# Kernel optimization log

Hardware: AMD Instinct MI355X
Metric: run time of the kernel (lower is better)

The kernel has to match this reference:

```python
import jax, jax.numpy as jnp
import numpy as np

NUM_RELS = 1315
FEAT_DIM = 768
RD = 32  # rel_emb_dim
OD = 32  # out_dim
B = 65536  # entities per side
NNZ = 1048576  # nonzeros per incidence matrix (avg degree 16)
EPS = 1e-12  # torch F.normalize eps


def _normalize(x):
    n = jnp.linalg.norm(x, axis=1, keepdims=True)
    return x / jnp.maximum(n, EPS)


def _agg(rows, cols, vals, rel_emb):
    # sparse.mm(inc, rel_emb): gather rel rows, scale, scatter-add to entities -> [B, RD]
    return jax.ops.segment_sum(vals[:, None] * rel_emb[cols], rows, num_segments=B)


def _entity_emb(ri, ci, vi, ro, co, vo, feat, rel_emb, W_in, b_in, W_out, b_out, W_ent, b_ent):
    in_emb = _agg(ri, ci, vi, rel_emb) @ W_in.T + b_in
    out_emb = _agg(ro, co, vo, rel_emb) @ W_out.T + b_out
    f = jnp.concatenate([feat, in_emb, out_emb], axis=1)  # [B, FEAT+2*RD]
    return _normalize(f @ W_ent.T + b_ent)


def setup_inputs() -> dict:
    key = jax.random.key(0)
    ks = iter(jax.random.split(key, 40))
    d = {}
    for p in ("h", "pos_t", "neg_t"):
        for s in ("in", "out"):
            d[f"{p}_{s}_rows"] = jax.random.randint(next(ks), (NNZ,), 0, B, dtype=jnp.int32)
            d[f"{p}_{s}_cols"] = jax.random.randint(next(ks), (NNZ,), 0, NUM_RELS, dtype=jnp.int32)
            d[f"{p}_{s}_vals"] = jax.random.uniform(next(ks), (NNZ,), dtype=jnp.float32)
        d[f"{p}_node_feat"] = jax.random.normal(next(ks), (B, FEAT_DIM), dtype=jnp.float32)
    d["eid"] = jax.random.randint(next(ks), (B,), 0, NUM_RELS, dtype=jnp.int32)
    # learned parameters
    d["rel_emb"] = jax.random.normal(next(ks), (NUM_RELS, RD), dtype=jnp.float32) * 0.02
    d["W_in"] = jax.random.normal(next(ks), (RD, RD), dtype=jnp.float32) * 0.1
    d["b_in"] = jnp.zeros((RD,), dtype=jnp.float32)
    d["W_out"] = jax.random.normal(next(ks), (RD, RD), dtype=jnp.float32) * 0.1
    d["b_out"] = jnp.zeros((RD,), dtype=jnp.float32)
    d["W_ent"] = jax.random.normal(next(ks), (OD, FEAT_DIM + 2 * RD), dtype=jnp.float32) * 0.02
    d["b_ent"] = jnp.zeros((OD,), dtype=jnp.float32)
    d["W_rel"] = jax.random.normal(next(ks), (OD, RD), dtype=jnp.float32) * 0.1
    d["b_rel"] = jnp.zeros((OD,), dtype=jnp.float32)
    return d


def reference(h_in_rows, h_in_cols, h_in_vals, h_out_rows, h_out_cols, h_out_vals, h_node_feat,
              pos_t_in_rows, pos_t_in_cols, pos_t_in_vals, pos_t_out_rows, pos_t_out_cols, pos_t_out_vals, pos_t_node_feat,
              neg_t_in_rows, neg_t_in_cols, neg_t_in_vals, neg_t_out_rows, neg_t_out_cols, neg_t_out_vals, neg_t_node_feat,
              eid, rel_emb, W_in, b_in, W_out, b_out, W_ent, b_ent, W_rel, b_rel):
    r_emb = _normalize(rel_emb[eid] @ W_rel.T + b_rel)  # [B, OD]
    h_emb = _entity_emb(h_in_rows, h_in_cols, h_in_vals, h_out_rows, h_out_cols, h_out_vals,
                        h_node_feat, rel_emb, W_in, b_in, W_out, b_out, W_ent, b_ent)
    pos_t_emb = _entity_emb(pos_t_in_rows, pos_t_in_cols, pos_t_in_vals, pos_t_out_rows, pos_t_out_cols, pos_t_out_vals,
                            pos_t_node_feat, rel_emb, W_in, b_in, W_out, b_out, W_ent, b_ent)
    neg_t_emb = _entity_emb(neg_t_in_rows, neg_t_in_cols, neg_t_in_vals, neg_t_out_rows, neg_t_out_cols, neg_t_out_vals,
                            neg_t_node_feat, rel_emb, W_in, b_in, W_out, b_out, W_ent, b_ent)
    pos_score = jnp.linalg.norm(h_emb + r_emb - pos_t_emb, axis=1)
    neg_score = jnp.linalg.norm(h_emb + r_emb - neg_t_emb, axis=1)
    return (pos_score, neg_score)
```

## Files before the change

### kernel.cpp

```cpp
#include <hip/hip_runtime.h>
#include <math.h>

#define N_RELS 1315
#define NB 65536
#define NNZV (1 << 20)
#define FEATD 768

#define NBUK 256
#define CAP  4608
#define CHUNK 4096
#define STG  2048
#define EPT  8
#define FPT  9

typedef float f32x4 __attribute__((ext_vector_type(4)));
typedef short s16x8 __attribute__((ext_vector_type(8)));
typedef float v2f  __attribute__((ext_vector_type(2)));

struct Mats { const int* rows[6]; const int* cols[6]; const float* vals[6]; };

__device__ __forceinline__ short f2bf(float f) {
    return __builtin_bit_cast(short, (__bf16)f);
}

__global__ void k_prep(const float* __restrict__ rel_emb,
                       const float* __restrict__ W_in, const float* __restrict__ b_in,
                       const float* __restrict__ W_out, const float* __restrict__ b_out,
                       const float* __restrict__ W_ent, const float* __restrict__ b_ent,
                       const float* __restrict__ W_rel, const float* __restrict__ b_rel,
                       float* __restrict__ Pcat, float* __restrict__ Prel,
                       float* __restrict__ bprime, unsigned* __restrict__ cursor)
{
    __shared__ float C[2][32][33];
    const int tid = threadIdx.x;
    if (cursor != nullptr && blockIdx.x < 6) {
        const int i = blockIdx.x * 256 + tid;
        cursor[i] = (unsigned)i * CAP;
    }
    for (int idx = tid; idx < 2 * 32 * 32; idx += 256) {
        int d = idx >> 10, o = (idx >> 5) & 31, t = idx & 31;
        const float* W  = d ? W_out : W_in;
        const float* we = W_ent + o * 832 + 768 + d * 32;
        float s = 0.f;
        #pragma unroll
        for (int j = 0; j < 32; ++j) s += we[j] * W[j * 32 + t];
        C[d][o][t] = s;
    }
    __syncthreads();

    const int row8 = blockIdx.x * 8 + (tid >> 5);
    const int o = tid & 31;
    if (row8 < 2 * N_RELS) {
        const int d = (row8 >= N_RELS) ? 1 : 0;
        const int r = row8 - d * N_RELS;
        const float* re = rel_emb + r * 32;
        float s = 0.f;
        #pragma unroll
        for (int t = 0; t < 32; ++t) s += re[t] * C[d][o][t];
        Pcat[row8 * 32 + o] = s;
    } else if (row8 < 3 * N_RELS) {
        const int r = row8 - 2 * N_RELS;
        const float* re = rel_emb + r * 32;
        float s = b_rel[o];
        #pragma unroll
        for (int j = 0; j < 32; ++j) s += W_rel[o * 32 + j] * re[j];
        float sq = s * s;
        #pragma unroll
        for (int m = 16; m; m >>= 1) sq += __shfl_xor(sq, m);
        Prel[r * 32 + o] = s / fmaxf(sqrtf(sq), 1e-12f);
    }
    if (blockIdx.x == 0 && tid < 32) {
        float s = b_ent[tid];
        #pragma unroll
        for (int j = 0; j < 32; ++j)
            s += b_in[j] * W_ent[tid * 832 + 768 + j] + b_out[j] * W_ent[tid * 832 + 800 + j];
        bprime[tid] = s;
    }
}

__global__ void k_wfrag(const float* __restrict__ W_ent, s16x8* __restrict__ wsB)
{
    const int t = blockIdx.x * 256 + threadIdx.x;
    if (t >= 24 * 2 * 64) return;
    const int kk = t >> 7, rem = t & 127, nt = rem >> 6, l = rem & 63;
    const int col = nt * 16 + (l & 15);
    const int k0  = kk * 32 + ((l >> 4) << 3);
    const float* w = W_ent + col * 832 + k0;
    s16x8 v;
    #pragma unroll
    for (int e = 0; e < 8; ++e) v[e] = f2bf(w[e]);
    wsB[t] = v;
}

__global__ __launch_bounds__(256) void k_bin(Mats m, uint2* __restrict__ bins,
                                             unsigned* __restrict__ cursor)
{
    __shared__ unsigned lcnt[NBUK];
    __shared__ unsigned gbase[NBUK];
    const int mm    = blockIdx.x >> 8;
    const int chunk = blockIdx.x & 255;
    const int tid   = threadIdx.x;
    const int* __restrict__ R = m.rows[mm];
    const int* __restrict__ C = m.cols[mm];
    const float* __restrict__ V = m.vals[mm];
    const int base = chunk * CHUNK;

    for (int st = 0; st < CHUNK / STG; ++st) {
        for (int i = tid; i < NBUK; i += 256) lcnt[i] = 0;
        __syncthreads();
        unsigned meta[EPT]; float val[EPT]; unsigned short lrank[EPT]; unsigned char buk[EPT];
        #pragma unroll
        for (int e = 0; e < EPT; ++e) {
            const int idx = base + st * STG + e * 256 + tid;
            const int row = R[idx];
            const int col = C[idx];
            val[e]  = V[idx];
            buk[e]  = (unsigned char)(row >> 8);
            meta[e] = ((unsigned)(row & 255) << 11) | (unsigned)col;
            lrank[e] = (unsigned short)atomicAdd(&lcnt[buk[e]], 1u);
        }
        __syncthreads();
        gbase[tid] = atomicAdd(&cursor[mm * NBUK + tid], lcnt[tid]);
        __syncthreads();
        #pragma unroll
        for (int e = 0; e < EPT; ++e)
            bins[gbase[buk[e]] + lrank[e]] = make_uint2(meta[e], __float_as_uint(val[e]));
        __syncthreads();
    }
}

__global__ __launch_bounds__(512) void k_fuse(const uint2* __restrict__ bins,
                                              const unsigned* __restrict__ cursor,
                                              const float* __restrict__ Pcat,
                                              float* __restrict__ aggY)
{
    __shared__ uint2 stage[CAP];
    __shared__ int hist[256], sc[256], ofs[256];
    const int set = blockIdx.x >> 8;
    const int b   = blockIdx.x & 255;
    const int t   = threadIdx.x;
    const int row  = t >> 1;
    const int half = t & 1;

    float acc[16];
    #pragma unroll
    for (int j = 0; j < 16; ++j) acc[j] = 0.f;

    for (int dir = 0; dir < 2; ++dir) {
        const int mb = (set * 2 + dir) * NBUK + b;
        const unsigned segbase = (unsigned)mb * CAP;
        const uint2* __restrict__ seg = bins + segbase;
        const int len = (int)(cursor[mb] - segbase);
        const float* __restrict__ P = Pcat + (size_t)dir * N_RELS * 32;

        if (t < 256) hist[t] = 0;
        __syncthreads();

        uint2 e[FPT];
        #pragma unroll
        for (int j = 0; j < FPT; ++j) {
            const int i = t + j * 512;
            if (i < len) e[j] = seg[i];
        }
        #pragma unroll
        for (int j = 0; j < FPT; ++j) {
            const int i = t + j * 512;
            if (i < len) atomicAdd(&hist[e[j].x >> 11], 1);
        }
        __syncthreads();

        if (t < 256) sc[t] = hist[t];
        __syncthreads();
        for (int off = 1; off < 256; off <<= 1) {
            const int x = (t >= off && t < 256) ? sc[t - off] : 0;
            __syncthreads();
            if (t < 256) sc[t] += x;
            __syncthreads();
        }
        if (t < 256) ofs[t] = t ? sc[t - 1] : 0;
        __syncthreads();
        const int myo = row ? sc[row - 1] : 0;
        const int myc = hist[row];

        #pragma unroll
        for (int j = 0; j < FPT; ++j) {
            const int i = t + j * 512;
            if (i < len) {
                const int pos = atomicAdd(&ofs[e[j].x >> 11], 1);
                stage[pos] = make_uint2(e[j].x & 2047u, e[j].y);
            }
        }
        __syncthreads();

        uint2 ed = (myc > 0) ? stage[myo] : make_uint2(0u, 0u);
        for (int j = 0; j < myc; ++j) {
            const uint2 nxt = (j + 1 < myc) ? stage[myo + j + 1] : make_uint2(0u, 0u);
            const float v = __uint_as_float(ed.y);
            const float4* prow = reinterpret_cast<const float4*>(P + (ed.x << 5) + half * 16);
            float4 p[4];
            #pragma unroll
            for (int q = 0; q < 4; ++q) p[q] = prow[q];
            #pragma unroll
            for (int q = 0; q < 4; ++q) {
                acc[q * 4 + 0] += v * p[q].x; acc[q * 4 + 1] += v * p[q].y;
                acc[q * 4 + 2] += v * p[q].z; acc[q * 4 + 3] += v * p[q].w;
            }
            ed = nxt;
        }
        __syncthreads();
    }

    float4* dst = reinterpret_cast<float4*>(
        aggY + ((size_t)set * NB + (size_t)b * 256 + row) * 32 + half * 16);
    #pragma unroll
    for (int q = 0; q < 4; ++q) {
        float4 wv;
        wv.x = acc[q * 4 + 0]; wv.y = acc[q * 4 + 1];
        wv.z = acc[q * 4 + 2]; wv.w = acc[q * 4 + 3];
        dst[q] = wv;
    }
}

__global__ void k_scatter(const int* __restrict__ rows, const int* __restrict__ cols,
                          const float* __restrict__ vals,
                          const float* __restrict__ Ptab, float* __restrict__ accs)
{
    const int stride = gridDim.x * blockDim.x;
    const int total = NNZV << 4;
    for (int g = blockIdx.x * blockDim.x + threadIdx.x; g < total; g += stride) {
        const int c2 = (g & 15) << 1;
        const int i  = g >> 4;
        const int row = rows[i];
        const int col = cols[i];
        const float v = vals[i];
        const float* p = Ptab + (col << 5) + c2;
        const int dst = (row << 5) + c2;
#if defined(__has_builtin) && __has_builtin(__builtin_amdgcn_global_atomic_fadd_v2f32)
        typedef __attribute__((address_space(1))) v2f* v2f_as1;
        v2f pv; pv.x = v * p[0]; pv.y = v * p[1];
        __builtin_amdgcn_global_atomic_fadd_v2f32(
            (v2f_as1)(unsigned long long)(accs + dst), pv);
#else
        atomicAdd(accs + dst,     v * p[0]);
        atomicAdd(accs + dst + 1, v * p[1]);
#endif
    }
}

__global__ __launch_bounds__(512, 4) void k_gemm(
    const float* __restrict__ feat_h, const float* __restrict__ feat_p,
    const float* __restrict__ feat_n,
    const s16x8* __restrict__ wsB, const float* __restrict__ bprime,
    const float* __restrict__ aggY, const int* __restrict__ eid,
    const float* __restrict__ Prel, float* __restrict__ out)
{
    __shared__ float4 lA[2][128 * 17];
    __shared__ float  lbp[32];

    const int tid  = threadIdx.x;
    const int lane = tid & 63;
    const int w    = tid >> 6;
    const int bid  = blockIdx.x;
    const int tile = (bid & 7) * 64 + (bid >> 3);
    const int e0   = tile << 7;

    const int l15 = lane & 15;
    const int kq  = lane >> 4;

    if (tid < 32) lbp[tid] = bprime[tid];

    const int srow = tid >> 4;
    const int scol = tid & 15;
    const s16x8* wsl = wsB + lane;
    const int rowA = (w << 4) + l15;

    f32x4 aH0 = {0.f,0.f,0.f,0.f}, aH1 = {0.f,0.f,0.f,0.f};
    f32x4 aP0 = {0.f,0.f,0.f,0.f}, aP1 = {0.f,0.f,0.f,0.f};
    f32x4 aN0 = {0.f,0.f,0.f,0.f}, aN1 = {0.f,0.f,0.f,0.f};

#define GEMM_SET(FEATP, A0, A1) do { \
    const float4* gs0 = reinterpret_cast<const float4*>((FEATP) + (size_t)(e0 + srow)      * FEATD) + scol; \
    const float4* gs1 = reinterpret_cast<const float4*>((FEATP) + (size_t)(e0 + 32 + srow) * FEATD) + scol; \
    const float4* gs2 = reinterpret_cast<const float4*>((FEATP) + (size_t)(e0 + 64 + srow) * FEATD) + scol; \
    const float4* gs3 = reinterpret_cast<const float4*>((FEATP) + (size_t)(e0 + 96 + srow) * FEATD) + scol; \
    float4 r0 = gs0[0], r1 = gs1[0], r2 = gs2[0], r3 = gs3[0]; \
    lA[0][(srow     ) * 17 + scol] = r0; \
    lA[0][(srow + 32) * 17 + scol] = r1; \
    lA[0][(srow + 64) * 17 + scol] = r2; \
    lA[0][(srow + 96) * 17 + scol] = r3; \
    r0 = gs0[16]; r1 = gs1[16]; r2 = gs2[16]; r3 = gs3[16]; \
    __syncthreads(); \
    for (int c = 0; c < 12; ++c) { \
        if (c < 11) { \
            lA[(c + 1) & 1][(srow     ) * 17 + scol] = r0; \
            lA[(c + 1) & 1][(srow + 32) * 17 + scol] = r1; \
            lA[(c + 1) & 1][(srow + 64) * 17 + scol] = r2; \
            lA[(c + 1) & 1][(srow + 96) * 17 + scol] = r3; \
            if (c < 10) { \
                r0 = gs0[(c + 2) * 16]; r1 = gs1[(c + 2) * 16]; \
                r2 = gs2[(c + 2) * 16]; r3 = gs3[(c + 2) * 16]; \
            } \
        } \
        _Pragma("unroll") \
        for (int s = 0; s < 2; ++s) { \
            const int kk = c * 2 + s; \
            const float4 fa0 = lA[c & 1][rowA * 17 + s * 8 + kq * 2]; \
            const float4 fa1 = lA[c & 1][rowA * 17 + s * 8 + kq * 2 + 1]; \
            s16x8 av; \
            av[0] = f2bf(fa0.x); av[1] = f2bf(fa0.y); av[2] = f2bf(fa0.z); av[3] = f2bf(fa0.w); \
            av[4] = f2bf(fa1.x); av[5] = f2bf(fa1.y); av[6] = f2bf(fa1.z); av[7] = f2bf(fa1.w); \
            const s16x8 wb0 = wsl[(kk * 2 + 0) << 6]; \
            const s16x8 wb1 = wsl[(kk * 2 + 1) << 6]; \
            A0 = __builtin_amdgcn_mfma_f32_16x16x32_bf16(av, wb0, A0, 0, 0, 0); \
            A1 = __builtin_amdgcn_mfma_f32_16x16x32_bf16(av, wb1, A1, 0, 0, 0); \
        } \
        __syncthreads(); \
    } \
} while (0)

    GEMM_SET(feat_h, aH0, aH1);
    GEMM_SET(feat_p, aP0, aP1);
    GEMM_SET(feat_n, aN0, aN1);

#undef GEMM_SET

    const float bp0 = lbp[l15], bp1 = lbp[l15 + 16];
    const int rbase = e0 + (w << 4) + (kq << 2);

#define NORM1(A0_, A1_, SOFF, Y0_, Y1_) do { \
    float v0 = (A0_)[e] + bp0 + aggY[(SOFF) + eoff + l15]; \
    float v1 = (A1_)[e] + bp1 + aggY[(SOFF) + eoff + l15 + 16]; \
    float sq = v0 * v0 + v1 * v1; \
    sq += __shfl_xor(sq, 1); sq += __shfl_xor(sq, 2); \
    sq += __shfl_xor(sq, 4); sq += __shfl_xor(sq, 8); \
    const float inv = 1.f / fmaxf(sqrtf(sq), 1e-12f); \
    Y0_ = v0 * inv; Y1_ = v1 * inv; \
} while (0)

    #pragma unroll
    for (int e = 0; e < 4; ++e) {
        const int ent = rbase + e;
        const size_t eoff = (size_t)ent * 32;
        float yh0, yh1, yp0, yp1, yn0, yn1;
        NORM1(aH0, aH1, (size_t)0,           yh0, yh1);
        NORM1(aP0, aP1, (size_t)NB * 32,     yp0, yp1);
        NORM1(aN0, aN1, (size_t)2 * NB * 32, yn0, yn1);
        const int ev = eid[ent];
        const float r0 = Prel[(size_t)ev * 32 + l15];
        const float r1 = Prel[(size_t)ev * 32 + l15 + 16];
        const float dp0 = yh0 + r0 - yp0, dp1 = yh1 + r1 - yp1;
        const float dn0 = yh0 + r0 - yn0, dn1 = yh1 + r1 - yn1;
        float sp = dp0 * dp0 + dp1 * dp1;
        float sn = dn0 * dn0 + dn1 * dn1;
        sp += __shfl_xor(sp, 1); sn += __shfl_xor(sn, 1);
        sp += __shfl_xor(sp, 2); sn += __shfl_xor(sn, 2);
        sp += __shfl_xor(sp, 4); sn += __shfl_xor(sn, 4);
        sp += __shfl_xor(sp, 8); sn += __shfl_xor(sn, 8);
        if (l15 == 0) { out[ent] = sqrtf(sp); out[NB + ent] = sqrtf(sn); }
    }
#undef NORM1
}

extern "C" void kernel_launch(void* const* d_in, const int* in_sizes, int n_in,
                              void* d_out, int out_size, void* d_ws, size_t ws_size,
                              hipStream_t stream)
{
    const float* feat_h = (const float*)d_in[6];
    const float* feat_p = (const float*)d_in[13];
    const float* feat_n = (const float*)d_in[20];
    const int*   eid    = (const int*)d_in[21];
    const float* rel_emb = (const float*)d_in[22];
    const float* W_in  = (const float*)d_in[23];
    const float* b_in  = (const float*)d_in[24];
    const float* W_out = (const float*)d_in[25];
    const float* b_out = (const float*)d_in[26];
    const float* W_ent = (const float*)d_in[27];
    const float* b_ent = (const float*)d_in[28];
    const float* W_rel = (const float*)d_in[29];
    const float* b_rel = (const float*)d_in[30];

    char* ws = (char*)d_ws;
    const size_t AGG_B   = (size_t)3 * NB * 32 * 4;
    const size_t BINS_B  = (size_t)6 * NBUK * CAP * 8;
    const size_t CURS_B  = 8192;
    const size_t PCAT_B  = (size_t)2 * N_RELS * 32 * 4;
    const size_t PREL_B  = (size_t)N_RELS * 32 * 4;
    const size_t BPR_B   = 128;
    const size_t WSB_B   = (size_t)24 * 2 * 64 * 16;
    const bool fast = ws_size >= AGG_B + BINS_B + CURS_B
                                + PCAT_B + PREL_B + BPR_B + WSB_B;

    float* aggY = (float*)ws;
    size_t off = AGG_B;
    uint2* bins = nullptr; unsigned* cursor = nullptr;
    if (fast) {
        bins   = (uint2*)(ws + off);    off += BINS_B;
        cursor = (unsigned*)(ws + off); off += CURS_B;
    }
    float* Pcat   = (float*)(ws + off); off += PCAT_B;
    float* Prel   = (float*)(ws + off); off += PREL_B;
    float* bprime = (float*)(ws + off); off += BPR_B;
    s16x8* wsB    = (s16x8*)(ws + off);

    k_prep<<<(3 * N_RELS + 7) / 8, 256, 0, stream>>>(rel_emb, W_in, b_in, W_out, b_out,
                                                     W_ent, b_ent, W_rel, b_rel,
                                                     Pcat, Prel, bprime, cursor);
    k_wfrag<<<12, 256, 0, stream>>>(W_ent, wsB);

    static const int base_idx[6] = {0, 3, 7, 10, 14, 17};
    if (fast) {
        Mats m;
        for (int i = 0; i < 6; ++i) {
            m.rows[i] = (const int*)d_in[base_idx[i]];
            m.cols[i] = (const int*)d_in[base_idx[i] + 1];
            m.vals[i] = (const float*)d_in[base_idx[i] + 2];
        }
        k_bin<<<6 * 256, 256, 0, stream>>>(m, bins, cursor);
        k_fuse<<<3 * 256, 512, 0, stream>>>(bins, cursor, Pcat, aggY);
    } else {
        hipMemsetAsync(aggY, 0, AGG_B, stream);
        for (int mm = 0; mm < 6; ++mm) {
            const int d = mm & 1, s = mm >> 1;
            k_scatter<<<32768, 256, 0, stream>>>((const int*)d_in[base_idx[mm]],
                                                 (const int*)d_in[base_idx[mm] + 1],
                                                 (const float*)d_in[base_idx[mm] + 2],
                                                 Pcat + (size_t)d * N_RELS * 32,
                                                 aggY + (size_t)s * NB * 32);
        }
    }

    k_gemm<<<512, 512, 0, stream>>>(feat_h, feat_p, feat_n, wsB, bprime,
                                    aggY, eid, Prel, (float*)d_out);
}
```

Before: 282.0 us.

## Co-schedule binning with feature GEMM in one kernel; split epilogue out

The binning pass and the dense feature GEMM now run in a single launch, interleaved three bin blocks to one GEMM block, so the latency-bound scatter-binning overlaps with the bandwidth-heavy feature GEMM. The GEMM writes its partial projections into aggY, k_fuse then adds the sparse aggregation on top, and a new light epilogue kernel does bias, normalization and scoring. This removes the separate GEMM stage after aggregation. In exchange aggY makes an extra read/write round trip, there is one more launch, and the bin blocks now use 512 threads with a GEMM-sized shared allocation, which may lower their occupancy.

New measurement: 428.2 us. +51.9%, slower.

```diff
diff --git a/kernel.cpp b/kernel.cpp
--- a/kernel.cpp
+++ b/kernel.cpp
@@ -8,9 +8,6 @@
 
 #define NBUK 256
 #define CAP  4608
-#define CHUNK 4096
-#define STG  2048
-#define EPT  8
 #define FPT  9
 
 typedef float f32x4 __attribute__((ext_vector_type(4)));
@@ -92,26 +89,35 @@
     wsB[t] = v;
 }
 
-__global__ __launch_bounds__(256) void k_bin(Mats m, uint2* __restrict__ bins,
-                                             unsigned* __restrict__ cursor)
-{
-    __shared__ unsigned lcnt[NBUK];
-    __shared__ unsigned gbase[NBUK];
-    const int mm    = blockIdx.x >> 8;
-    const int chunk = blockIdx.x & 255;
-    const int tid   = threadIdx.x;
-    const int* __restrict__ R = m.rows[mm];
-    const int* __restrict__ C = m.cols[mm];
-    const float* __restrict__ V = m.vals[mm];
-    const int base = chunk * CHUNK;
-
-    for (int st = 0; st < CHUNK / STG; ++st) {
-        for (int i = tid; i < NBUK; i += 256) lcnt[i] = 0;
-        __syncthreads();
-        unsigned meta[EPT]; float val[EPT]; unsigned short lrank[EPT]; unsigned char buk[EPT];
-        #pragma unroll
-        for (int e = 0; e < EPT; ++e) {
-            const int idx = base + st * STG + e * 256 + tid;
+__global__ __launch_bounds__(512, 4) void k_mix(
+    Mats m, uint2* __restrict__ bins, unsigned* __restrict__ cursor,
+    const float* __restrict__ feat_h, const float* __restrict__ feat_p,
+    const float* __restrict__ feat_n,
+    const s16x8* __restrict__ wsB, float* __restrict__ aggY)
+{
+    __shared__ float4 lA[2][128 * 17];
+
+    const int b   = blockIdx.x;
+    const int tid = threadIdx.x;
+
+    if ((b & 3) != 3) {
+        if (bins == nullptr) return;
+        unsigned* lcnt  = reinterpret_cast<unsigned*>(&lA[0][0]);
+        unsigned* gbase = lcnt + 256;
+        const int bi    = (b >> 2) * 3 + (b & 3);
+        const int mm    = bi >> 8;
+        const int chunk = bi & 255;
+        const int* __restrict__ R = m.rows[mm];
+        const int* __restrict__ C = m.cols[mm];
+        const float* __restrict__ V = m.vals[mm];
+        const int base = chunk * 4096;
+
+        if (tid < 256) lcnt[tid] = 0;
+        __syncthreads();
+        unsigned meta[8]; float val[8]; unsigned short lrank[8]; unsigned char buk[8];
+        #pragma unroll
+        for (int e = 0; e < 8; ++e) {
+            const int idx = base + e * 512 + tid;
             const int row = R[idx];
             const int col = C[idx];
             val[e]  = V[idx];
@@ -120,155 +126,22 @@
             lrank[e] = (unsigned short)atomicAdd(&lcnt[buk[e]], 1u);
         }
         __syncthreads();
-        gbase[tid] = atomicAdd(&cursor[mm * NBUK + tid], lcnt[tid]);
-        __syncthreads();
-        #pragma unroll
-        for (int e = 0; e < EPT; ++e)
+        if (tid < 256) gbase[tid] = atomicAdd(&cursor[mm * NBUK + tid], lcnt[tid]);
+        __syncthreads();
+        #pragma unroll
+        for (int e = 0; e < 8; ++e)
             bins[gbase[buk[e]] + lrank[e]] = make_uint2(meta[e], __float_as_uint(val[e]));
-        __syncthreads();
-    }
-}
-
-__global__ __launch_bounds__(512) void k_fuse(const uint2* __restrict__ bins,
-                                              const unsigned* __restrict__ cursor,
-                                              const float* __restrict__ Pcat,
-                                              float* __restrict__ aggY)
-{
-    __shared__ uint2 stage[CAP];
-    __shared__ int hist[256], sc[256], ofs[256];
-    const int set = blockIdx.x >> 8;
-    const int b   = blockIdx.x & 255;
-    const int t   = threadIdx.x;
-    const int row  = t >> 1;
-    const int half = t & 1;
-
-    float acc[16];
-    #pragma unroll
-    for (int j = 0; j < 16; ++j) acc[j] = 0.f;
-
-    for (int dir = 0; dir < 2; ++dir) {
-        const int mb = (set * 2 + dir) * NBUK + b;
-        const unsigned segbase = (unsigned)mb * CAP;
-        const uint2* __restrict__ seg = bins + segbase;
-        const int len = (int)(cursor[mb] - segbase);
-        const float* __restrict__ P = Pcat + (size_t)dir * N_RELS * 32;
-
-        if (t < 256) hist[t] = 0;
-        __syncthreads();
-
-        uint2 e[FPT];
-        #pragma unroll
-        for (int j = 0; j < FPT; ++j) {
-            const int i = t + j * 512;
-            if (i < len) e[j] = seg[i];
-        }
-        #pragma unroll
-        for (int j = 0; j < FPT; ++j) {
-            const int i = t + j * 512;
-            if (i < len) atomicAdd(&hist[e[j].x >> 11], 1);
-        }
-        __syncthreads();
-
-        if (t < 256) sc[t] = hist[t];
-        __syncthreads();
-        for (int off = 1; off < 256; off <<= 1) {
-            const int x = (t >= off && t < 256) ? sc[t - off] : 0;
-            __syncthreads();
-            if (t < 256) sc[t] += x;
-            __syncthreads();
-        }
-        if (t < 256) ofs[t] = t ? sc[t - 1] : 0;
-        __syncthreads();
-        const int myo = row ? sc[row - 1] : 0;
-        const int myc = hist[row];
-
-        #pragma unroll
-        for (int j = 0; j < FPT; ++j) {
-            const int i = t + j * 512;
-            if (i < len) {
-                const int pos = atomicAdd(&ofs[e[j].x >> 11], 1);
-                stage[pos] = make_uint2(e[j].x & 2047u, e[j].y);
-            }
-        }
-        __syncthreads();
-
-        uint2 ed = (myc > 0) ? stage[myo] : make_uint2(0u, 0u);
-        for (int j = 0; j < myc; ++j) {
-            const uint2 nxt = (j + 1 < myc) ? stage[myo + j + 1] : make_uint2(0u, 0u);
-            const float v = __uint_as_float(ed.y);
-            const float4* prow = reinterpret_cast<const float4*>(P + (ed.x << 5) + half * 16);
-            float4 p[4];
-            #pragma unroll
-            for (int q = 0; q < 4; ++q) p[q] = prow[q];
-            #pragma unroll
-            for (int q = 0; q < 4; ++q) {
-                acc[q * 4 + 0] += v * p[q].x; acc[q * 4 + 1] += v * p[q].y;
-                acc[q * 4 + 2] += v * p[q].z; acc[q * 4 + 3] += v * p[q].w;
-            }
-            ed = nxt;
-        }
-        __syncthreads();
-    }
-
-    float4* dst = reinterpret_cast<float4*>(
-        aggY + ((size_t)set * NB + (size_t)b * 256 + row) * 32 + half * 16);
-    #pragma unroll
-    for (int q = 0; q < 4; ++q) {
-        float4 wv;
-        wv.x = acc[q * 4 + 0]; wv.y = acc[q * 4 + 1];
-        wv.z = acc[q * 4 + 2]; wv.w = acc[q * 4 + 3];
-        dst[q] = wv;
-    }
-}
-
-__global__ void k_scatter(const int* __restrict__ rows, const int* __restrict__ cols,
-                          const float* __restrict__ vals,
-                          const float* __restrict__ Ptab, float* __restrict__ accs)
-{
-    const int stride = gridDim.x * blockDim.x;
-    const int total = NNZV << 4;
-    for (int g = blockIdx.x * blockDim.x + threadIdx.x; g < total; g += stride) {
-        const int c2 = (g & 15) << 1;
-        const int i  = g >> 4;
-        const int row = rows[i];
-        const int col = cols[i];
-        const float v = vals[i];
-        const float* p = Ptab + (col << 5) + c2;
-        const int dst = (row << 5) + c2;
-#if defined(__has_builtin) && __has_builtin(__builtin_amdgcn_global_atomic_fadd_v2f32)
-        typedef __attribute__((address_space(1))) v2f* v2f_as1;
-        v2f pv; pv.x = v * p[0]; pv.y = v * p[1];
-        __builtin_amdgcn_global_atomic_fadd_v2f32(
-            (v2f_as1)(unsigned long long)(accs + dst), pv);
-#else
-        atomicAdd(accs + dst,     v * p[0]);
-        atomicAdd(accs + dst + 1, v * p[1]);
-#endif
-    }
-}
-
-__global__ __launch_bounds__(512, 4) void k_gemm(
-    const float* __restrict__ feat_h, const float* __restrict__ feat_p,
-    const float* __restrict__ feat_n,
-    const s16x8* __restrict__ wsB, const float* __restrict__ bprime,
-    const float* __restrict__ aggY, const int* __restrict__ eid,
-    const float* __restrict__ Prel, float* __restrict__ out)
-{
-    __shared__ float4 lA[2][128 * 17];
-    __shared__ float  lbp[32];
-
-    const int tid  = threadIdx.x;
+        return;
+    }
+
+    const int g    = b >> 2;
     const int lane = tid & 63;
     const int w    = tid >> 6;
-    const int bid  = blockIdx.x;
-    const int tile = (bid & 7) * 64 + (bid >> 3);
+    const int tile = (g & 7) * 64 + (g >> 3);
     const int e0   = tile << 7;
 
     const int l15 = lane & 15;
     const int kq  = lane >> 4;
-
-    if (tid < 32) lbp[tid] = bprime[tid];
-
     const int srow = tid >> 4;
     const int scol = tid & 15;
     const s16x8* wsl = wsB + lane;
@@ -324,41 +197,166 @@
 
 #undef GEMM_SET
 
-    const float bp0 = lbp[l15], bp1 = lbp[l15 + 16];
     const int rbase = e0 + (w << 4) + (kq << 2);
-
-#define NORM1(A0_, A1_, SOFF, Y0_, Y1_) do { \
-    float v0 = (A0_)[e] + bp0 + aggY[(SOFF) + eoff + l15]; \
-    float v1 = (A1_)[e] + bp1 + aggY[(SOFF) + eoff + l15 + 16]; \
-    float sq = v0 * v0 + v1 * v1; \
-    sq += __shfl_xor(sq, 1); sq += __shfl_xor(sq, 2); \
-    sq += __shfl_xor(sq, 4); sq += __shfl_xor(sq, 8); \
-    const float inv = 1.f / fmaxf(sqrtf(sq), 1e-12f); \
-    Y0_ = v0 * inv; Y1_ = v1 * inv; \
-} while (0)
-
     #pragma unroll
     for (int e = 0; e < 4; ++e) {
-        const int ent = rbase + e;
-        const size_t eoff = (size_t)ent * 32;
-        float yh0, yh1, yp0, yp1, yn0, yn1;
-        NORM1(aH0, aH1, (size_t)0,           yh0, yh1);
-        NORM1(aP0, aP1, (size_t)NB * 32,     yp0, yp1);
-        NORM1(aN0, aN1, (size_t)2 * NB * 32, yn0, yn1);
-        const int ev = eid[ent];
-        const float r0 = Prel[(size_t)ev * 32 + l15];
-        const float r1 = Prel[(size_t)ev * 32 + l15 + 16];
-        const float dp0 = yh0 + r0 - yp0, dp1 = yh1 + r1 - yp1;
-        const float dn0 = yh0 + r0 - yn0, dn1 = yh1 + r1 - yn1;
-        float sp = dp0 * dp0 + dp1 * dp1;
-        float sn = dn0 * dn0 + dn1 * dn1;
-        sp += __shfl_xor(sp, 1); sn += __shfl_xor(sn, 1);
-        sp += __shfl_xor(sp, 2); sn += __shfl_xor(sn, 2);
-        sp += __shfl_xor(sp, 4); sn += __shfl_xor(sn, 4);
-        sp += __shfl_xor(sp, 8); sn += __shfl_xor(sn, 8);
-        if (l15 == 0) { out[ent] = sqrtf(sp); out[NB + ent] = sqrtf(sn); }
-    }
-#undef NORM1
+        const size_t eoff = (size_t)(rbase + e) * 32;
+        aggY[eoff + l15]                         = aH0[e];
+        aggY[eoff + l15 + 16]                    = aH1[e];
+        aggY[(size_t)NB * 32 + eoff + l15]       = aP0[e];
+        aggY[(size_t)NB * 32 + eoff + l15 + 16]  = aP1[e];
+        aggY[(size_t)2 * NB * 32 + eoff + l15]      = aN0[e];
+        aggY[(size_t)2 * NB * 32 + eoff + l15 + 16] = aN1[e];
+    }
+}
+
+__global__ __launch_bounds__(512) void k_fuse(const uint2* __restrict__ bins,
+                                              const unsigned* __restrict__ cursor,
+                                              const float* __restrict__ Pcat,
+                                              float* __restrict__ aggY)
+{
+    __shared__ uint2 stage[CAP];
+    __shared__ int hist[256], sc[256], ofs[256];
+    const int set = blockIdx.x >> 8;
+    const int b   = blockIdx.x & 255;
+    const int t   = threadIdx.x;
+    const int row  = t >> 1;
+    const int half = t & 1;
+
+    float acc[16];
+    #pragma unroll
+    for (int j = 0; j < 16; ++j) acc[j] = 0.f;
+
+    for (int dir = 0; dir < 2; ++dir) {
+        const int mb = (set * 2 + dir) * NBUK + b;
+        const unsigned segbase = (unsigned)mb * CAP;
+        const uint2* __restrict__ seg = bins + segbase;
+        const int len = (int)(cursor[mb] - segbase);
+        const float* __restrict__ P = Pcat + (size_t)dir * N_RELS * 32;
+
+        if (t < 256) hist[t] = 0;
+        __syncthreads();
+
+        uint2 e[FPT];
+        #pragma unroll
+        for (int j = 0; j < FPT; ++j) {
+            const int i = t + j * 512;
+            if (i < len) e[j] = seg[i];
+        }
+        #pragma unroll
+        for (int j = 0; j < FPT; ++j) {
+            const int i = t + j * 512;
+            if (i < len) atomicAdd(&hist[e[j].x >> 11], 1);
+        }
+        __syncthreads();
+
+        if (t < 256) sc[t] = hist[t];
+        __syncthreads();
+        for (int off = 1; off < 256; off <<= 1) {
+            const int x = (t >= off && t < 256) ? sc[t - off] : 0;
+            __syncthreads();
+            if (t < 256) sc[t] += x;
+            __syncthreads();
+        }
+        if (t < 256) ofs[t] = t ? sc[t - 1] : 0;
+        __syncthreads();
+        const int myo = row ? sc[row - 1] : 0;
+        const int myc = hist[row];
+
+        #pragma unroll
+        for (int j = 0; j < FPT; ++j) {
+            const int i = t + j * 512;
+            if (i < len) {
+                const int pos = atomicAdd(&ofs[e[j].x >> 11], 1);
+                stage[pos] = make_uint2(e[j].x & 2047u, e[j].y);
+            }
+        }
+        __syncthreads();
+
+        uint2 ed = (myc > 0) ? stage[myo] : make_uint2(0u, 0u);
+        for (int j = 0; j < myc; ++j) {
+            const uint2 nxt = (j + 1 < myc) ? stage[myo + j + 1] : make_uint2(0u, 0u);
+            const float v = __uint_as_float(ed.y);
+            const float4* prow = reinterpret_cast<const float4*>(P + (ed.x << 5) + half * 16);
+            float4 p[4];
+            #pragma unroll
+            for (int q = 0; q < 4; ++q) p[q] = prow[q];
+            #pragma unroll
+            for (int q = 0; q < 4; ++q) {
+                acc[q * 4 + 0] += v * p[q].x; acc[q * 4 + 1] += v * p[q].y;
+                acc[q * 4 + 2] += v * p[q].z; acc[q * 4 + 3] += v * p[q].w;
+            }
+            ed = nxt;
+        }
+        __syncthreads();
+    }
+
+    float4* dst = reinterpret_cast<float4*>(
+        aggY + ((size_t)set * NB + (size_t)b * 256 + row) * 32 + half * 16);
+    #pragma unroll
+    for (int q = 0; q < 4; ++q) {
+        const float4 old = dst[q];
+        float4 wv;
+        wv.x = acc[q * 4 + 0] + old.x; wv.y = acc[q * 4 + 1] + old.y;
+        wv.z = acc[q * 4 + 2] + old.z; wv.w = acc[q * 4 + 3] + old.w;
+        dst[q] = wv;
+    }
+}
+
+__global__ __launch_bounds__(256) void k_epi(const float* __restrict__ aggY,
+                                             const float* __restrict__ bprime,
+                                             const int* __restrict__ eid,
+                                             const float* __restrict__ Prel,
+                                             float* __restrict__ out)
+{
+    const int tid = blockIdx.x * 256 + threadIdx.x;
+    const int ent = tid >> 5;
+    const int c   = tid & 31;
+    const float bp = bprime[c];
+    float yh = aggY[(size_t)ent * 32 + c] + bp;
+    float yp = aggY[(size_t)NB * 32 + (size_t)ent * 32 + c] + bp;
+    float yn = aggY[(size_t)2 * NB * 32 + (size_t)ent * 32 + c] + bp;
+    float sh = yh * yh, sp2 = yp * yp, sn2 = yn * yn;
+    #pragma unroll
+    for (int m = 1; m <= 16; m <<= 1) {
+        sh += __shfl_xor(sh, m); sp2 += __shfl_xor(sp2, m); sn2 += __shfl_xor(sn2, m);
+    }
+    yh /= fmaxf(sqrtf(sh), 1e-12f);
+    yp /= fmaxf(sqrtf(sp2), 1e-12f);
+    yn /= fmaxf(sqrtf(sn2), 1e-12f);
+    const float r = Prel[(size_t)eid[ent] * 32 + c];
+    const float dp = yh + r - yp;
+    const float dn = yh + r - yn;
+    float sp = dp * dp, sn = dn * dn;
+    #pragma unroll
+    for (int m = 1; m <= 16; m <<= 1) { sp += __shfl_xor(sp, m); sn += __shfl_xor(sn, m); }
+    if (c == 0) { out[ent] = sqrtf(sp); out[NB + ent] = sqrtf(sn); }
+}
+
+__global__ void k_scatter(const int* __restrict__ rows, const int* __restrict__ cols,
+                          const float* __restrict__ vals,
+                          const float* __restrict__ Ptab, float* __restrict__ accs)
+{
+    const int stride = gridDim.x * blockDim.x;
+    const int total = NNZV << 4;
+    for (int g = blockIdx.x * blockDim.x + threadIdx.x; g < total; g += stride) {
+        const int c2 = (g & 15) << 1;
+        const int i  = g >> 4;
+        const int row = rows[i];
+        const int col = cols[i];
+        const float v = vals[i];
+        const float* p = Ptab + (col << 5) + c2;
+        const int dst = (row << 5) + c2;
+#if defined(__has_builtin) && __has_builtin(__builtin_amdgcn_global_atomic_fadd_v2f32)
+        typedef __attribute__((address_space(1))) v2f* v2f_as1;
+        v2f pv; pv.x = v * p[0]; pv.y = v * p[1];
+        __builtin_amdgcn_global_atomic_fadd_v2f32(
+            (v2f_as1)(unsigned long long)(accs + dst), pv);
+#else
+        atomicAdd(accs + dst,     v * p[0]);
+        atomicAdd(accs + dst + 1, v * p[1]);
+#endif
+    }
 }
 
 extern "C" void kernel_launch(void* const* d_in, const int* in_sizes, int n_in,
@@ -407,18 +405,19 @@
                                                      Pcat, Prel, bprime, cursor);
     k_wfrag<<<12, 256, 0, stream>>>(W_ent, wsB);
 
+    Mats m;
     static const int base_idx[6] = {0, 3, 7, 10, 14, 17};
+    for (int i = 0; i < 6; ++i) {
+        m.rows[i] = (const int*)d_in[base_idx[i]];
+        m.cols[i] = (const int*)d_in[base_idx[i] + 1];
+        m.vals[i] = (const float*)d_in[base_idx[i] + 2];
+    }
+
     if (fast) {
-        Mats m;
-        for (int i = 0; i < 6; ++i) {
-            m.rows[i] = (const int*)d_in[base_idx[i]];
-            m.cols[i] = (const int*)d_in[base_idx[i] + 1];
-            m.vals[i] = (const float*)d_in[base_idx[i] + 2];
-        }
-        k_bin<<<6 * 256, 256, 0, stream>>>(m, bins, cursor);
+        k_mix<<<2048, 512, 0, stream>>>(m, bins, cursor, feat_h, feat_p, feat_n, wsB, aggY);
         k_fuse<<<3 * 256, 512, 0, stream>>>(bins, cursor, Pcat, aggY);
     } else {
-        hipMemsetAsync(aggY, 0, AGG_B, stream);
+        k_mix<<<2048, 512, 0, stream>>>(m, nullptr, nullptr, feat_h, feat_p, feat_n, wsB, aggY);
         for (int mm = 0; mm < 6; ++mm) {
             const int d = mm & 1, s = mm >> 1;
             k_scatter<<<32768, 256, 0, stream>>>((const int*)d_in[base_idx[mm]],
@@ -429,6 +428,5 @@
         }
     }
 
-    k_gemm<<<512, 512, 0, stream>>>(feat_h, feat_p, feat_n, wsB, bprime,
-                                    aggY, eid, Prel, (float*)d_out);
-}
+    k_epi<<<8192, 256, 0, stream>>>(aggY, bprime, eid, Prel, (float*)d_out);
+}
```
